# Kernel tuning notes

Hardware: AMD Instinct MI355X
Metric: run time of the kernel (lower is better)

The kernel has to match this reference:

```python
import jax, jax.numpy as jnp
import numpy as np

N = 100_000          # nodes
E = 3_200_000        # edges (avg degree 32)
NEG_SLOPE = 0.2      # PyG GATConv default


def _gat_conv(x, src, dst, W, a_src, a_dst, b, n):
    """Single-head PyG-style GATConv. src/dst already include self-loops."""
    h = x @ W                                   # [N, F_out]
    logits = (h @ a_src)[src] + (h @ a_dst)[dst]  # [E']
    e = jax.nn.leaky_relu(logits, NEG_SLOPE)
    m = jax.ops.segment_max(e, dst, num_segments=n)
    ex = jnp.exp(e - m[dst])                    # stable ragged softmax over in-edges
    s = jax.ops.segment_sum(ex, dst, num_segments=n)
    alpha = ex / (s[dst] + 1e-16)
    out = jax.ops.segment_sum(h[src] * alpha[:, None], dst, num_segments=n)
    return out + b


def setup_inputs() -> dict:
    key = jax.random.key(0)
    ks = jax.random.split(key, 20)
    x = jax.random.normal(ks[0], (N, 3), dtype=jnp.float32)
    edge_index = jax.random.randint(ks[1], (2, E), 0, N, dtype=jnp.int64)

    def lin(k, fin, fout):
        return jax.random.normal(k, (fin, fout), dtype=jnp.float32) * (1.0 / np.sqrt(fin))

    def att(k, f):
        return jax.random.normal(k, (f,), dtype=jnp.float32) * (1.0 / np.sqrt(f))

    inp = {"x": x, "edge_index": edge_index}
    # forward-direction convs
    inp["W1"], inp["as1"], inp["ad1"], inp["b1"] = lin(ks[2], 3, 16), att(ks[3], 16), att(ks[4], 16), jnp.zeros((16,), jnp.float32)
    inp["W2"], inp["as2"], inp["ad2"], inp["b2"] = lin(ks[5], 16, 1), att(ks[6], 1), att(ks[7], 1), jnp.zeros((1,), jnp.float32)
    # reverse-direction convs
    inp["W1r"], inp["as1r"], inp["ad1r"], inp["b1r"] = lin(ks[8], 3, 16), att(ks[9], 16), att(ks[10], 16), jnp.zeros((16,), jnp.float32)
    inp["W2r"], inp["as2r"], inp["ad2r"], inp["b2r"] = lin(ks[11], 16, 1), att(ks[12], 1), att(ks[13], 1), jnp.zeros((1,), jnp.float32)
    return inp


def reference(x, edge_index, W1, as1, ad1, b1, W2, as2, ad2, b2,
              W1r, as1r, ad1r, b1r, W2r, as2r, ad2r, b2r):
    n = x.shape[0]
    loops = jnp.arange(n, dtype=edge_index.dtype)
    # forward direction (self-loops appended, as PyG add_self_loops=True)
    src = jnp.concatenate([edge_index[0], loops])
    dst = jnp.concatenate([edge_index[1], loops])
    # reverse direction: stack([ei[1], ei[0]]) then self-loops
    rsrc = jnp.concatenate([edge_index[1], loops])
    rdst = jnp.concatenate([edge_index[0], loops])

    xf = jax.nn.relu(_gat_conv(x, src, dst, W1, as1, ad1, b1, n))
    xf = _gat_conv(xf, src, dst, W2, as2, ad2, b2, n)

    xr = jax.nn.relu(_gat_conv(x, rsrc, rdst, W1r, as1r, ad1r, b1r, n))
    xr = _gat_conv(xr, rsrc, rdst, W2r, as2r, ad2r, b2r, n)

    return (xf + xr) * 0.5
```

## Files before the change

### kernel.cpp

```cpp
#include <hip/hip_runtime.h>
#include <math.h>

#define NSLOPE 0.2f
#define BSH 8
#define BNODES 256
#define NID_MASK 0x1FFFF
#define SENT 0xFFFFFFFFu
#define CAP 10240
#define GB 512
#define RE 2048
#define SLOT 12
#define SPILLCAP 256
#define BAGT 1024
#define CPT (CAP / BAGT)

__device__ __forceinline__ float lrelu(float v) { return v > 0.f ? v : NSLOPE * v; }

__global__ void k_flag(const unsigned long long* __restrict__ p, int* __restrict__ flag) {
    int t = threadIdx.x;
    bool bad = false;
#pragma unroll
    for (int i = 0; i < 4; i++)
        if (p[t * 4 + i] >= (1ull << 32)) bad = true;
    unsigned long long mask = __ballot(bad);
    if (t == 0) *flag = (mask == 0ull) ? 1 : 0;
}

__global__ void k_prep(const float* __restrict__ x,
                       const float* __restrict__ as1, const float* __restrict__ ad1,
                       const float* __restrict__ as1r, const float* __restrict__ ad1r,
                       const float* __restrict__ W1, const float* __restrict__ W1r,
                       float4* __restrict__ rec4f, float4* __restrict__ rec4r,
                       float* __restrict__ s1df, float* __restrict__ s1dr,
                       int* __restrict__ gcur, int NS, int N) {
    int i = blockIdx.x * blockDim.x + threadIdx.x;
    if (i < NS) gcur[i] = 0;
    if (i >= N) return;
    float x0 = x[3 * i], x1 = x[3 * i + 1], x2 = x[3 * i + 2];
    float ssf = 0.f, sdf = 0.f, ssr = 0.f, sdr = 0.f;
#pragma unroll
    for (int k = 0; k < 16; k++) {
        float hf = x0 * W1[k] + x1 * W1[16 + k] + x2 * W1[32 + k];
        ssf += hf * as1[k];
        sdf += hf * ad1[k];
        float hr = x0 * W1r[k] + x1 * W1r[16 + k] + x2 * W1r[32 + k];
        ssr += hr * as1r[k];
        sdr += hr * ad1r[k];
    }
    rec4f[i] = make_float4(x0, x1, x2, ssf);
    rec4r[i] = make_float4(x0, x1, x2, ssr);
    s1df[i] = sdf; s1dr[i] = sdr;
}

__global__ void __launch_bounds__(512) k_scatsort(
        const void* __restrict__ ei, long long E, const int* __restrict__ flag,
        int NB, int NS, int* __restrict__ gcur, unsigned* __restrict__ bin) {
    extern __shared__ unsigned smem[];
    unsigned* slots = smem;
    int* cnt  = (int*)(slots + (size_t)NS * SLOT);
    int* gpos = cnt + NS;
    int* spill_s = gpos + NS;
    int* spill_p = spill_s + SPILLCAP;
    unsigned* spill_r = (unsigned*)(spill_p + SPILLCAP);
    int* spn = (int*)(spill_r + SPILLCAP);

    int t = threadIdx.x;
    int fl = *flag;
    long long chunk = (E + GB - 1) / GB;
    long long cstart = (long long)blockIdx.x * chunk;
    long long cend = cstart + chunk; if (cend > E) cend = E;

    for (long long rs = cstart; rs < cend; rs += RE) {
        int ne = (int)min((long long)RE, cend - rs);
        for (int c = t; c < NS; c += 512) cnt[c] = 0;
        if (t == 0) *spn = 0;
        __syncthreads();
#pragma unroll
        for (int k = 0; k < RE / 512; k++) {
            int idx = t + k * 512;
            if (idx < ne) {
                long long i = rs + idx;
                int u, v;
                if (fl) { const long long* p = (const long long*)ei; u = (int)p[i]; v = (int)p[E + i]; }
                else    { const int* p = (const int*)ei; u = p[i]; v = p[E + i]; }
                unsigned r0 = (unsigned)u | ((unsigned)(v & (BNODES - 1)) << 17);
                int s0 = v >> BSH;
                unsigned r1 = (unsigned)v | ((unsigned)(u & (BNODES - 1)) << 17);
                int s1 = NB + (u >> BSH);
                int p0 = atomicAdd(&cnt[s0], 1);
                if (p0 < SLOT) slots[s0 * SLOT + p0] = r0;
                else { int sp = atomicAdd(spn, 1); if (sp < SPILLCAP) { spill_s[sp] = s0; spill_p[sp] = p0; spill_r[sp] = r0; } }
                int p1 = atomicAdd(&cnt[s1], 1);
                if (p1 < SLOT) slots[s1 * SLOT + p1] = r1;
                else { int sp = atomicAdd(spn, 1); if (sp < SPILLCAP) { spill_s[sp] = s1; spill_p[sp] = p1; spill_r[sp] = r1; } }
            }
        }
        __syncthreads();
        for (int c = t; c < NS; c += 512) {
            int n = cnt[c];
            int rn = (n + 1) & ~1;
            gpos[c] = rn ? atomicAdd(&gcur[c], rn) : 0;
        }
        __syncthreads();
        for (int c = t; c < NS; c += 512) {
            int n = cnt[c];
            if (!n) continue;
            int rn = (n + 1) & ~1;
            int g = gpos[c];
            long long b = (long long)c * CAP;
            int m = n < SLOT ? n : SLOT;
            if (g + rn <= CAP) {
                uint2* bp = (uint2*)(bin + b + g);
                int np = (m + 1) >> 1;
                for (int j = 0; j < np; j++) {
                    unsigned v0 = slots[c * SLOT + 2 * j];
                    unsigned v1 = (2 * j + 1 < m) ? slots[c * SLOT + 2 * j + 1] : SENT;
                    bp[j] = make_uint2(v0, v1);
                }
                if (n > SLOT && rn > n)
                    bin[b + g + n] = SENT;
            }
        }
        int nsp = *spn; if (nsp > SPILLCAP) nsp = SPILLCAP;
        for (int i = t; i < nsp; i += 512) {
            int s = spill_s[i];
            int off = gpos[s] + spill_p[i];
            if (off < CAP) bin[(long long)s * CAP + off] = spill_r[i];
        }
        __syncthreads();
    }
}

__global__ void __launch_bounds__(BAGT) k_bagg1(
        unsigned* __restrict__ bin, const int* __restrict__ gcur,
        const float4* __restrict__ rec4f, const float* __restrict__ s1df,
        const float4* __restrict__ rec4r, const float* __restrict__ s1dr,
        const float* __restrict__ b1, const float* __restrict__ W1,
        const float* __restrict__ W2,
        const float* __restrict__ as2, const float* __restrict__ ad2,
        const float* __restrict__ b1r, const float* __restrict__ W1r,
        const float* __restrict__ W2r,
        const float* __restrict__ as2r, const float* __restrict__ ad2r,
        float2* __restrict__ p2f, float* __restrict__ s2df,
        float2* __restrict__ p2r, float* __restrict__ s2dr,
        int* __restrict__ aoff, int* __restrict__ aend, int NB, int N) {
    int bb = blockIdx.x, dir = blockIdx.y;
    const float4* rec4 = dir ? rec4r : rec4f;
    const float* s1d = dir ? s1dr : s1df;
    const float* b1_ = dir ? b1r : b1;
    const float* W1_ = dir ? W1r : W1;
    const float* W2_ = dir ? W2r : W2;
    float as2v = dir ? as2r[0] : as2[0];
    float ad2v = dir ? ad2r[0] : ad2[0];
    float2* p2 = dir ? p2r : p2f;
    float* s2d = dir ? s2dr : s2df;

    int c = dir * NB + bb;
    long long base = (long long)c * CAP;
    int n = gcur[c]; if (n > CAP) n = CAP;
    int v0 = bb << BSH;
    int nv = N - v0; if (nv > BNODES) nv = BNODES;

    __shared__ int cnt[BNODES];
    __shared__ int loff[BNODES];
    __shared__ int segtot[4];
    __shared__ unsigned lds_u[CAP];
    int t = threadIdx.x;

    unsigned recs[CPT];
#pragma unroll
    for (int k = 0; k < CPT; k++) {
        int i = t + k * BAGT;
        recs[k] = (i < n) ? __builtin_nontemporal_load(bin + base + i) : SENT;
    }
    if (t < BNODES) cnt[t] = 0;
    __syncthreads();
#pragma unroll
    for (int k = 0; k < CPT; k++)
        if (recs[k] != SENT) atomicAdd(&cnt[recs[k] >> 17], 1);
    __syncthreads();
    if (t < BNODES) {
        int lane = t & 63, w = t >> 6;
        int val = cnt[t];
        int incl = val;
#pragma unroll
        for (int od = 1; od < 64; od <<= 1) {
            int up = __shfl_up(incl, od);
            if (lane >= od) incl += up;
        }
        if (lane == 63) segtot[w] = incl;
        loff[t] = incl - val;
    }
    __syncthreads();
    if (t < BNODES) {
        int w = t >> 6;
        int offs = 0;
#pragma unroll
        for (int j = 0; j < 4; j++) offs += (j < w) ? segtot[j] : 0;
        int ex = loff[t] + offs;
        loff[t] = ex;
        cnt[t] = ex;
    }
    __syncthreads();
#pragma unroll
    for (int k = 0; k < CPT; k++)
        if (recs[k] != SENT) {
            int p = atomicAdd(&cnt[recs[k] >> 17], 1);
            lds_u[p] = recs[k] & NID_MASK;
        }
    __syncthreads();
    int node = t >> 2, lane = t & 3;
    float sdv = (node < nv) ? s1d[v0 + node] : 0.f;
    float d = 0.f, a0 = 0.f, a1 = 0.f, a2 = 0.f;
    if (node < nv) {
        int ls = loff[node], le = cnt[node];
        for (int pos = ls + lane; pos < le; pos += 4) {
            unsigned u = lds_u[pos];
            float4 r = rec4[u];
            float w = __expf(lrelu(r.w + sdv));
            d += w; a0 += w * r.x; a1 += w * r.y; a2 += w * r.z;
        }
    }
#pragma unroll
    for (int mask = 1; mask < 4; mask <<= 1) {
        d  += __shfl_xor(d, mask);
        a0 += __shfl_xor(a0, mask);
        a1 += __shfl_xor(a1, mask);
        a2 += __shfl_xor(a2, mask);
    }
    if (lane == 0 && node < nv) {
        int v = v0 + node;
        float4 r = rec4[v];
        float w = __expf(lrelu(r.w + sdv));
        float dd = d + w;
        float inv = 1.f / (dd + 1e-16f);
        float m0 = (a0 + w * r.x) * inv;
        float m1 = (a1 + w * r.y) * inv;
        float m2 = (a2 + w * r.z) * inv;
        float h2v = 0.f;
#pragma unroll
        for (int k = 0; k < 16; k++) {
            float o = m0 * W1_[k] + m1 * W1_[16 + k] + m2 * W1_[32 + k] + b1_[k];
            o = fmaxf(o, 0.f);
            h2v += o * W2_[k];
        }
        p2[v] = make_float2(h2v, h2v * as2v);
        s2d[v] = h2v * ad2v;
    }
    int nreal = (nv > 0) ? cnt[nv - 1] : 0;
    for (int i = t; i < nreal; i += BAGT) bin[base + i] = lds_u[i];
    if (t < nv) {
        aoff[dir * N + v0 + t] = (int)(base + loff[t]);
        aend[dir * N + v0 + t] = (int)(base + cnt[t]);
    }
}

__global__ void k_agg2(const unsigned* __restrict__ bin,
                       const int* __restrict__ aoff, const int* __restrict__ aend,
                       const float2* __restrict__ p2f, const float* __restrict__ s2df,
                       const float2* __restrict__ p2r, const float* __restrict__ s2dr,
                       const float* __restrict__ b2, const float* __restrict__ b2r,
                       float* __restrict__ out, int N) {
    int tid = blockIdx.x * blockDim.x + threadIdx.x;
    int v = tid >> 3;
    int lane = tid & 7;
    if (v >= N) return;
    float res[2];
#pragma unroll
    for (int dir = 0; dir < 2; dir++) {
        const float2* p2 = dir ? p2r : p2f;
        const float* s2d = dir ? s2dr : s2df;
        float bias = dir ? b2r[0] : b2[0];
        float sd = s2d[v];
        int st = aoff[dir * N + v], en = aend[dir * N + v];
        float d = 0.f, a = 0.f;
        if (lane == 0) {
            float2 ts = p2[v];
            float w = __expf(lrelu(ts.y + sd));
            d = w; a = w * ts.x;
        }
        int j = st + lane;
        for (; j + 24 < en; j += 32) {
            unsigned u0 = __builtin_nontemporal_load(bin + j);
            unsigned u1 = __builtin_nontemporal_load(bin + j + 8);
            unsigned u2 = __builtin_nontemporal_load(bin + j + 16);
            unsigned u3 = __builtin_nontemporal_load(bin + j + 24);
            float2 t0 = p2[u0];
            float2 t1 = p2[u1];
            float2 t2 = p2[u2];
            float2 t3 = p2[u3];
            float w0 = __expf(lrelu(t0.y + sd));
            float w1 = __expf(lrelu(t1.y + sd));
            float w2 = __expf(lrelu(t2.y + sd));
            float w3 = __expf(lrelu(t3.y + sd));
            d += (w0 + w1) + (w2 + w3);
            a += w0 * t0.x + w1 * t1.x + w2 * t2.x + w3 * t3.x;
        }
        for (; j < en; j += 8) {
            unsigned u = __builtin_nontemporal_load(bin + j);
            float2 t = p2[u];
            float w = __expf(lrelu(t.y + sd));
            d += w;
            a += w * t.x;
        }
#pragma unroll
        for (int mask = 1; mask < 8; mask <<= 1) {
            d += __shfl_xor(d, mask);
            a += __shfl_xor(a, mask);
        }
        res[dir] = a / (d + 1e-16f) + bias;
    }
    if (lane == 0) out[v] = 0.5f * (res[0] + res[1]);
}

extern "C" void kernel_launch(void* const* d_in, const int* in_sizes, int n_in,
                              void* d_out, int out_size, void* d_ws, size_t ws_size,
                              hipStream_t stream) {
    const float* x   = (const float*)d_in[0];
    const void*  ei  = d_in[1];
    const float* W1  = (const float*)d_in[2];
    const float* as1 = (const float*)d_in[3];
    const float* ad1 = (const float*)d_in[4];
    const float* b1  = (const float*)d_in[5];
    const float* W2  = (const float*)d_in[6];
    const float* as2 = (const float*)d_in[7];
    const float* ad2 = (const float*)d_in[8];
    const float* b2  = (const float*)d_in[9];
    const float* W1r  = (const float*)d_in[10];
    const float* as1r = (const float*)d_in[11];
    const float* ad1r = (const float*)d_in[12];
    const float* b1r  = (const float*)d_in[13];
    const float* W2r  = (const float*)d_in[14];
    const float* as2r = (const float*)d_in[15];
    const float* ad2r = (const float*)d_in[16];
    const float* b2r  = (const float*)d_in[17];

    const int N = in_sizes[0] / 3;
    const long long E = in_sizes[1] / 2;
    const int NB = (N + BNODES - 1) >> BSH;
    const int NS = 2 * NB;

    char* w = (char*)d_ws;
    size_t o = 0;
    auto A = [&](size_t bytes) { o = (o + 255) & ~(size_t)255; size_t r = o; o += bytes; return r; };
    size_t oFlag = A(64);
    size_t oR4f  = A(sizeof(float4) * N);
    size_t oR4r  = A(sizeof(float4) * N);
    size_t oS1df = A(sizeof(float) * N);
    size_t oS1dr = A(sizeof(float) * N);
    size_t oP2f  = A(sizeof(float2) * N);
    size_t oS2df = A(sizeof(float) * N);
    size_t oP2r  = A(sizeof(float2) * N);
    size_t oS2dr = A(sizeof(float) * N);
    size_t oAoff = A(sizeof(int) * 2 * N);
    size_t oAend = A(sizeof(int) * 2 * N);
    size_t oGcur = A(sizeof(int) * NS);
    size_t oBin  = A(sizeof(unsigned) * (size_t)NS * CAP);
    (void)ws_size; (void)n_in; (void)out_size;

    int*    flag = (int*)(w + oFlag);
    float4* rec4f = (float4*)(w + oR4f);
    float4* rec4r = (float4*)(w + oR4r);
    float*  s1df = (float*)(w + oS1df);
    float*  s1dr = (float*)(w + oS1dr);
    float2* p2f  = (float2*)(w + oP2f);
    float*  s2df = (float*)(w + oS2df);
    float2* p2r  = (float2*)(w + oP2r);
    float*  s2dr = (float*)(w + oS2dr);
    int*    aoff = (int*)(w + oAoff);
    int*    aend = (int*)(w + oAend);
    int*    gcur = (int*)(w + oGcur);
    unsigned* bin = (unsigned*)(w + oBin);

    dim3 gN((N + 255) / 256);
    dim3 gAgg1(NB, 2);
    dim3 gAgg2((N * 8 + 255) / 256);

    size_t smem = sizeof(unsigned) * (size_t)NS * SLOT
                + sizeof(int) * (size_t)NS * 2
                + sizeof(int) * SPILLCAP * 2
                + sizeof(unsigned) * SPILLCAP
                + 64;

    k_flag<<<1, 64, 0, stream>>>((const unsigned long long*)ei, flag);
    k_prep<<<gN, 256, 0, stream>>>(x, as1, ad1, as1r, ad1r, W1, W1r,
                                   rec4f, rec4r, s1df, s1dr, gcur, NS, N);
    k_scatsort<<<GB, 512, smem, stream>>>(ei, E, flag, NB, NS, gcur, bin);
    k_bagg1<<<gAgg1, BAGT, 0, stream>>>(bin, gcur, rec4f, s1df, rec4r, s1dr,
                                        b1, W1, W2, as2, ad2,
                                        b1r, W1r, W2r, as2r, ad2r,
                                        p2f, s2df, p2r, s2dr, aoff, aend, NB, N);
    k_agg2<<<gAgg2, 256, 0, stream>>>(bin, aoff, aend, p2f, s2df, p2r, s2dr,
                                      b2, b2r, (float*)d_out, N);
}
```

Baseline: 250.8 us.

## Fold flag check into scatter, vectorize bin I/O, halve aggregation block size

Removes the separate k_flag launch: every scatter block now recomputes the 64-bit/32-bit index check itself into shared memory. Raises the scatter grid from 512 to 1536 blocks and the per-round edge chunk from 2048 to 2560. In k_bagg1 the block shrinks from 1024 to 512 threads, bucket records are read and written back as uint2 pairs, and each node is handled by 2 lanes instead of 4. The aim is to cut launch overhead and the number of memory transactions, at the cost of redundant flag reads per block and less parallelism per node; reading only n>>1 pairs may drop the last record when a bucket count is odd.

```diff
diff --git a/kernel.cpp b/kernel.cpp
--- a/kernel.cpp
+++ b/kernel.cpp
@@ -7,24 +7,14 @@
 #define NID_MASK 0x1FFFF
 #define SENT 0xFFFFFFFFu
 #define CAP 10240
-#define GB 512
-#define RE 2048
+#define GB 1536
+#define RE 2560
 #define SLOT 12
 #define SPILLCAP 256
-#define BAGT 1024
-#define CPT (CAP / BAGT)
+#define BAGT 512
+#define CPP (CAP / (2 * BAGT))
 
 __device__ __forceinline__ float lrelu(float v) { return v > 0.f ? v : NSLOPE * v; }
-
-__global__ void k_flag(const unsigned long long* __restrict__ p, int* __restrict__ flag) {
-    int t = threadIdx.x;
-    bool bad = false;
-#pragma unroll
-    for (int i = 0; i < 4; i++)
-        if (p[t * 4 + i] >= (1ull << 32)) bad = true;
-    unsigned long long mask = __ballot(bad);
-    if (t == 0) *flag = (mask == 0ull) ? 1 : 0;
-}
 
 __global__ void k_prep(const float* __restrict__ x,
                        const float* __restrict__ as1, const float* __restrict__ ad1,
@@ -53,7 +43,7 @@
 }
 
 __global__ void __launch_bounds__(512) k_scatsort(
-        const void* __restrict__ ei, long long E, const int* __restrict__ flag,
+        const void* __restrict__ ei, long long E,
         int NB, int NS, int* __restrict__ gcur, unsigned* __restrict__ bin) {
     extern __shared__ unsigned smem[];
     unsigned* slots = smem;
@@ -63,9 +53,20 @@
     int* spill_p = spill_s + SPILLCAP;
     unsigned* spill_r = (unsigned*)(spill_p + SPILLCAP);
     int* spn = (int*)(spill_r + SPILLCAP);
+    __shared__ int flagsm;
 
     int t = threadIdx.x;
-    int fl = *flag;
+    if (t < 64) {
+        const unsigned long long* p = (const unsigned long long*)ei;
+        bool bad = false;
+#pragma unroll
+        for (int i = 0; i < 4; i++)
+            if (p[t * 4 + i] >= (1ull << 32)) bad = true;
+        unsigned long long mask = __ballot(bad);
+        if (t == 0) flagsm = (mask == 0ull) ? 1 : 0;
+    }
+    __syncthreads();
+    int fl = flagsm;
     long long chunk = (E + GB - 1) / GB;
     long long cstart = (long long)blockIdx.x * chunk;
     long long cend = cstart + chunk; if (cend > E) cend = E;
@@ -158,6 +159,7 @@
     int c = dir * NB + bb;
     long long base = (long long)c * CAP;
     int n = gcur[c]; if (n > CAP) n = CAP;
+    int npair = n >> 1;
     int v0 = bb << BSH;
     int nv = N - v0; if (nv > BNODES) nv = BNODES;
 
@@ -167,17 +169,20 @@
     __shared__ unsigned lds_u[CAP];
     int t = threadIdx.x;
 
-    unsigned recs[CPT];
-#pragma unroll
-    for (int k = 0; k < CPT; k++) {
+    uint2 recs[CPP];
+    const uint2* bp = (const uint2*)(bin + base);
+#pragma unroll
+    for (int k = 0; k < CPP; k++) {
         int i = t + k * BAGT;
-        recs[k] = (i < n) ? __builtin_nontemporal_load(bin + base + i) : SENT;
+        recs[k] = (i < npair) ? bp[i] : make_uint2(SENT, SENT);
     }
     if (t < BNODES) cnt[t] = 0;
     __syncthreads();
 #pragma unroll
-    for (int k = 0; k < CPT; k++)
-        if (recs[k] != SENT) atomicAdd(&cnt[recs[k] >> 17], 1);
+    for (int k = 0; k < CPP; k++) {
+        if (recs[k].x != SENT) atomicAdd(&cnt[recs[k].x >> 17], 1);
+        if (recs[k].y != SENT) atomicAdd(&cnt[recs[k].y >> 17], 1);
+    }
     __syncthreads();
     if (t < BNODES) {
         int lane = t & 63, w = t >> 6;
@@ -203,31 +208,33 @@
     }
     __syncthreads();
 #pragma unroll
-    for (int k = 0; k < CPT; k++)
-        if (recs[k] != SENT) {
-            int p = atomicAdd(&cnt[recs[k] >> 17], 1);
-            lds_u[p] = recs[k] & NID_MASK;
-        }
-    __syncthreads();
-    int node = t >> 2, lane = t & 3;
+    for (int k = 0; k < CPP; k++) {
+        if (recs[k].x != SENT) {
+            int p = atomicAdd(&cnt[recs[k].x >> 17], 1);
+            lds_u[p] = recs[k].x & NID_MASK;
+        }
+        if (recs[k].y != SENT) {
+            int p = atomicAdd(&cnt[recs[k].y >> 17], 1);
+            lds_u[p] = recs[k].y & NID_MASK;
+        }
+    }
+    __syncthreads();
+    int node = t >> 1, lane = t & 1;
     float sdv = (node < nv) ? s1d[v0 + node] : 0.f;
     float d = 0.f, a0 = 0.f, a1 = 0.f, a2 = 0.f;
     if (node < nv) {
         int ls = loff[node], le = cnt[node];
-        for (int pos = ls + lane; pos < le; pos += 4) {
+        for (int pos = ls + lane; pos < le; pos += 2) {
             unsigned u = lds_u[pos];
             float4 r = rec4[u];
             float w = __expf(lrelu(r.w + sdv));
             d += w; a0 += w * r.x; a1 += w * r.y; a2 += w * r.z;
         }
     }
-#pragma unroll
-    for (int mask = 1; mask < 4; mask <<= 1) {
-        d  += __shfl_xor(d, mask);
-        a0 += __shfl_xor(a0, mask);
-        a1 += __shfl_xor(a1, mask);
-        a2 += __shfl_xor(a2, mask);
-    }
+    d  += __shfl_xor(d, 1);
+    a0 += __shfl_xor(a0, 1);
+    a1 += __shfl_xor(a1, 1);
+    a2 += __shfl_xor(a2, 1);
     if (lane == 0 && node < nv) {
         int v = v0 + node;
         float4 r = rec4[v];
@@ -248,7 +255,12 @@
         s2d[v] = h2v * ad2v;
     }
     int nreal = (nv > 0) ? cnt[nv - 1] : 0;
-    for (int i = t; i < nreal; i += BAGT) bin[base + i] = lds_u[i];
+    if (t == 0 && (nreal & 1)) lds_u[nreal] = SENT;
+    __syncthreads();
+    int ndp = (nreal + 1) >> 1;
+    uint2* bq = (uint2*)(bin + base);
+    for (int i = t; i < ndp; i += BAGT)
+        bq[i] = make_uint2(lds_u[2 * i], lds_u[2 * i + 1]);
     if (t < nv) {
         aoff[dir * N + v0 + t] = (int)(base + loff[t]);
         aend[dir * N + v0 + t] = (int)(base + cnt[t]);
@@ -343,7 +355,6 @@
     char* w = (char*)d_ws;
     size_t o = 0;
     auto A = [&](size_t bytes) { o = (o + 255) & ~(size_t)255; size_t r = o; o += bytes; return r; };
-    size_t oFlag = A(64);
     size_t oR4f  = A(sizeof(float4) * N);
     size_t oR4r  = A(sizeof(float4) * N);
     size_t oS1df = A(sizeof(float) * N);
@@ -358,7 +369,6 @@
     size_t oBin  = A(sizeof(unsigned) * (size_t)NS * CAP);
     (void)ws_size; (void)n_in; (void)out_size;
 
-    int*    flag = (int*)(w + oFlag);
     float4* rec4f = (float4*)(w + oR4f);
     float4* rec4r = (float4*)(w + oR4r);
     float*  s1df = (float*)(w + oS1df);
@@ -382,10 +392,9 @@
                 + sizeof(unsigned) * SPILLCAP
                 + 64;
 
-    k_flag<<<1, 64, 0, stream>>>((const unsigned long long*)ei, flag);
     k_prep<<<gN, 256, 0, stream>>>(x, as1, ad1, as1r, ad1r, W1, W1r,
                                    rec4f, rec4r, s1df, s1dr, gcur, NS, N);
-    k_scatsort<<<GB, 512, smem, stream>>>(ei, E, flag, NB, NS, gcur, bin);
+    k_scatsort<<<GB, 512, smem, stream>>>(ei, E, NB, NS, gcur, bin);
     k_bagg1<<<gAgg1, BAGT, 0, stream>>>(bin, gcur, rec4f, s1df, rec4r, s1dr,
                                         b1, W1, W2, as2, ad2,
                                         b1r, W1r, W2r, as2r, ad2r,
```

Result: faster. 240.8 us (-4.0%).
